# Kernel optimization log

Measured on AMD Instinct MI355X. Metric: run time of the kernel, lower is better.

Reference implementation:

```python
import jax, jax.numpy as jnp
import numpy as np

ALPHA = 0.1
K = 10


def setup_inputs() -> dict:
    key = jax.random.key(0)
    k1, k2, k3, k4, k5, k6 = jax.random.split(key, 6)
    N, F_in, H = 100000, 256, 128
    E, E_lp = 1600000, 400000
    return {
        "x": jax.random.normal(k1, (N, F_in), dtype=jnp.float32),
        "edge_index": jax.random.randint(k2, (2, E), 0, N, dtype=jnp.int64),
        "pos_edge_index": jax.random.randint(k3, (2, E_lp), 0, N, dtype=jnp.int64),
        "neg_edge_index": jax.random.randint(k4, (2, E_lp), 0, N, dtype=jnp.int64),
        "W1": jax.random.normal(k5, (F_in, H), dtype=jnp.float32) * (1.0 / np.sqrt(F_in)),
        "W2": jax.random.normal(k6, (H, H), dtype=jnp.float32) * (1.0 / np.sqrt(H)),
    }


def _appnp_propagate(h, src, dst, norm, num_nodes):
    # z_{k+1} = (1-alpha) * A_hat z_k + alpha * h   (K hops)
    z = h
    for _ in range(K):
        msg = norm[:, None] * z[src]                         # [E+N, d] gather
        agg = jax.ops.segment_sum(msg, dst, num_segments=num_nodes)  # scatter-add
        z = (1.0 - ALPHA) * agg + ALPHA * h
    return z


def reference(x, edge_index, pos_edge_index, neg_edge_index, W1, W2):
    N = x.shape[0]
    # add self-loops, GCN symmetric normalization: d^-1/2 A_sl d^-1/2
    loops = jnp.arange(N, dtype=edge_index.dtype)
    src = jnp.concatenate([edge_index[0], loops])
    dst = jnp.concatenate([edge_index[1], loops])
    deg = jax.ops.segment_sum(jnp.ones_like(dst, dtype=x.dtype), dst, num_segments=N)
    dinv = jax.lax.rsqrt(jnp.maximum(deg, 1.0))
    norm = dinv[src] * dinv[dst]

    # encode: two APPNP layers with ReLU in between (drop_rate = 0)
    z = _appnp_propagate(x @ W1, src, dst, norm, N)
    z = jax.nn.relu(z)
    z = _appnp_propagate(z @ W2, src, dst, norm, N)

    # decode: edge dot products over concatenated pos/neg edges
    e = jnp.concatenate([pos_edge_index, neg_edge_index], axis=-1)
    return jnp.sum(z[e[0]] * z[e[1]], axis=-1)
```

## Files before the change

### kernel.cpp

```cpp
#include <hip/hip_runtime.h>


constexpr int Hd = 128;
constexpr int Fin = 256;
constexpr float A_ = 0.1f;
constexpr float OMA = 0.9f;

typedef float vf2 __attribute__((ext_vector_type(2)));

__device__ __forceinline__ int idx_at(const void* p, size_t i, int is64) {
    if (is64) return (int)((const long long*)p)[i];
    return ((const int*)p)[i];
}

__device__ __forceinline__ unsigned pack_bf16x2(float x, float y) {
    unsigned ux = __float_as_uint(x);
    unsigned uy = __float_as_uint(y);
    ux = (ux + 0x7fffu + ((ux >> 16) & 1u)) >> 16;
    uy = (uy + 0x7fffu + ((uy >> 16) & 1u)) & 0xffff0000u;
    return ux | uy;
}

__device__ __forceinline__ float2 unpack_bf16x2(unsigned v) {
    float2 r;
    r.x = __uint_as_float(v << 16);
    r.y = __uint_as_float(v & 0xffff0000u);
    return r;
}

__device__ __forceinline__ unsigned short pack_fp8x2(float x, float y) {
    int v = __builtin_amdgcn_cvt_pk_fp8_f32(x, y, 0, false);
    return (unsigned short)(unsigned)v;
}

__device__ __forceinline__ float2 unpack_fp8x2(unsigned short v) {
    vf2 r = __builtin_amdgcn_cvt_pk_f32_fp8((int)(unsigned)v, false);
    float2 o;
    o.x = r[0];
    o.y = r[1];
    return o;
}

__global__ void k_detect(const int* __restrict__ p, int npairs, int* __restrict__ flag) {
    __shared__ int any32;
    if (threadIdx.x == 0) any32 = 0;
    __syncthreads();
    for (int i = threadIdx.x; i < npairs; i += blockDim.x)
        if (p[2 * i + 1] != 0) any32 = 1;
    __syncthreads();
    if (threadIdx.x == 0) *flag = any32 ? 0 : 1;
}


__global__ void k_zero_i32(int* __restrict__ p, int n) {
    int i = blockIdx.x * blockDim.x + threadIdx.x;
    if (i < n) p[i] = 0;
}

__global__ void k_count(const void* __restrict__ ei, int E, int* __restrict__ cnt,
                        const int* __restrict__ flag) {
    int is64 = *flag;
    int e = blockIdx.x * blockDim.x + threadIdx.x;
    if (e < E) {
        int d = idx_at(ei, (size_t)E + e, is64);
        atomicAdd(&cnt[d], 1);
    }
}

__global__ void k_dinv(const int* __restrict__ cnt, float* __restrict__ dinv, int N) {
    int i = blockIdx.x * blockDim.x + threadIdx.x;
    if (i < N) dinv[i] = rsqrtf((float)(cnt[i] + 1));
}

__global__ void k_scan1(const int* __restrict__ cnt, int* __restrict__ rp,
                        int* __restrict__ bsum, int N) {
    __shared__ int s[256];
    int t = threadIdx.x;
    int i = blockIdx.x * 256 + t;
    int v = (i < N) ? (cnt[i] + 1) : 0;
    s[t] = v;
    __syncthreads();
    for (int off = 1; off < 256; off <<= 1) {
        int add = (t >= off) ? s[t - off] : 0;
        __syncthreads();
        s[t] += add;
        __syncthreads();
    }
    if (i < N) rp[i] = s[t] - v;
    if (t == 255) bsum[blockIdx.x] = s[255];
}

__global__ void k_scan2(int* __restrict__ bsum, int nb) {
    __shared__ int s[512];
    int t = threadIdx.x;
    int v = (t < nb) ? bsum[t] : 0;
    s[t] = v;
    __syncthreads();
    for (int off = 1; off < 512; off <<= 1) {
        int add = (t >= off) ? s[t - off] : 0;
        __syncthreads();
        s[t] += add;
        __syncthreads();
    }
    if (t < nb) bsum[t] = s[t] - v;
}

__global__ void k_scan3(int* __restrict__ rp, const int* __restrict__ bsum,
                        int* __restrict__ cursor, const float* __restrict__ dinv,
                        int2* __restrict__ cw, int N, int Etot) {
    int i = blockIdx.x * blockDim.x + threadIdx.x;
    if (i < N) {
        int r = rp[i] + bsum[i >> 8];
        rp[i] = r;
        cursor[i] = 1;
        float d = dinv[i];
        int2 p;
        p.x = i;
        p.y = __float_as_int(OMA * d * d);
        cw[r] = p;
    }
    if (i == 0) rp[N] = Etot;
}

__global__ void k_place(const void* __restrict__ ei, int E,
                        const int* __restrict__ rp, int* __restrict__ cursor,
                        const float* __restrict__ dinv,
                        int2* __restrict__ cw, const int* __restrict__ flag) {
    int is64 = *flag;
    int e = blockIdx.x * blockDim.x + threadIdx.x;
    if (e < E) {
        int s = idx_at(ei, (size_t)e, is64);
        int d = idx_at(ei, (size_t)E + e, is64);
        int pos = rp[d] + atomicAdd(&cursor[d], 1);
        int2 p;
        p.x = s;
        p.y = __float_as_int(OMA * dinv[s] * dinv[d]);
        cw[pos] = p;
    }
}


template <int KTOT, bool RELU>
__global__ __launch_bounds__(256) void k_gemm(const float* __restrict__ A,
                                              const float* __restrict__ B,
                                              unsigned short* __restrict__ z0,
                                              unsigned* __restrict__ ah, int N) {
    __shared__ float As[64][36];
    __shared__ float Bs[32][128];
    const int t  = threadIdx.x;
    const int tx = t & 15;
    const int ty = t >> 4;
    const int r0 = blockIdx.x * 64;

    float acc[4][8];
#pragma unroll
    for (int i = 0; i < 4; ++i)
#pragma unroll
        for (int j = 0; j < 8; ++j) acc[i][j] = 0.f;

    for (int k0 = 0; k0 < KTOT; k0 += 32) {
#pragma unroll
        for (int p = 0; p < 2; ++p) {
            int row = p * 32 + (t >> 3);
            int kk  = (t & 7) * 4;
            int gr  = r0 + row;
            float4 v = make_float4(0.f, 0.f, 0.f, 0.f);
            if (gr < N) v = *(const float4*)&A[(size_t)gr * KTOT + k0 + kk];
            if (RELU) {
                v.x = fmaxf(v.x, 0.f); v.y = fmaxf(v.y, 0.f);
                v.z = fmaxf(v.z, 0.f); v.w = fmaxf(v.w, 0.f);
            }
            *(float4*)&As[row][kk] = v;
        }
#pragma unroll
        for (int p = 0; p < 4; ++p) {
            int kr = p * 8 + (t >> 5);
            int c  = (t & 31) * 4;
            *(float4*)&Bs[kr][c] = *(const float4*)&B[(size_t)(k0 + kr) * Hd + c];
        }
        __syncthreads();
#pragma unroll
        for (int kk = 0; kk < 32; ++kk) {
            float a[4];
#pragma unroll
            for (int i = 0; i < 4; ++i) a[i] = As[ty * 4 + i][kk];
            float4 b0 = *(const float4*)&Bs[kk][tx * 4];
            float4 b1 = *(const float4*)&Bs[kk][64 + tx * 4];
            float b[8] = {b0.x, b0.y, b0.z, b0.w, b1.x, b1.y, b1.z, b1.w};
#pragma unroll
            for (int i = 0; i < 4; ++i)
#pragma unroll
                for (int j = 0; j < 8; ++j) acc[i][j] = fmaf(a[i], b[j], acc[i][j]);
        }
        __syncthreads();
    }
#pragma unroll
    for (int i = 0; i < 4; ++i) {
        int gr = r0 + ty * 4 + i;
        if (gr < N) {
            ushort2 f0, f1;
            f0.x = pack_fp8x2(acc[i][0], acc[i][1]);
            f0.y = pack_fp8x2(acc[i][2], acc[i][3]);
            f1.x = pack_fp8x2(acc[i][4], acc[i][5]);
            f1.y = pack_fp8x2(acc[i][6], acc[i][7]);
            *(ushort2*)&z0[((size_t)gr << 6) + tx * 2]      = f0;
            *(ushort2*)&z0[((size_t)gr << 6) + 32 + tx * 2] = f1;
            uint2 a0, a1;
            a0.x = pack_bf16x2(A_ * acc[i][0], A_ * acc[i][1]);
            a0.y = pack_bf16x2(A_ * acc[i][2], A_ * acc[i][3]);
            a1.x = pack_bf16x2(A_ * acc[i][4], A_ * acc[i][5]);
            a1.y = pack_bf16x2(A_ * acc[i][6], A_ * acc[i][7]);
            *(uint2*)&ah[((size_t)gr << 6) + tx * 2]      = a0;
            *(uint2*)&ah[((size_t)gr << 6) + 32 + tx * 2] = a1;
        }
    }
}


template <int B, int IN8>
__device__ __forceinline__ void hop_batch(const void* __restrict__ zb,
                                          const int2* __restrict__ cw,
                                          int e, int lane,
                                          float& ax, float& ay,
                                          float& bx, float& by) {
    int2 p[B];
#pragma unroll
    for (int k = 0; k < B; ++k) p[k] = cw[e + k];
    unsigned zv[B];
#pragma unroll
    for (int k = 0; k < B; ++k) {
        if (IN8) zv[k] = ((const unsigned short*)zb)[((unsigned)p[k].x << 6) + lane];
        else     zv[k] = ((const unsigned*)zb)[((unsigned)p[k].x << 6) + lane];
    }
#pragma unroll
    for (int k = 0; k < B; ++k) {
        float wv = __int_as_float(p[k].y);
        float2 z = IN8 ? unpack_fp8x2((unsigned short)zv[k]) : unpack_bf16x2(zv[k]);
        if (k & 1) { bx = fmaf(wv, z.x, bx); by = fmaf(wv, z.y, by); }
        else       { ax = fmaf(wv, z.x, ax); ay = fmaf(wv, z.y, ay); }
    }
}

template <int IN8, int OUTM>
__global__ __launch_bounds__(256) void k_hop(const void* __restrict__ zin,
                                             const unsigned* __restrict__ ah,
                                             void* __restrict__ zout,
                                             const int* __restrict__ rp,
                                             const int2* __restrict__ cw, int N) {
    int wid  = (blockIdx.x * blockDim.x + threadIdx.x) >> 6;
    int lane = threadIdx.x & 63;
    if (wid >= N) return;

    int e   = __builtin_amdgcn_readfirstlane(rp[wid]);
    int end = __builtin_amdgcn_readfirstlane(rp[wid + 1]);

    float2 hh = unpack_bf16x2(ah[((size_t)wid << 6) + lane]);

    float ax = 0.f, ay = 0.f, bx = 0.f, by = 0.f;

    for (; e + 16 <= end; e += 16)
        hop_batch<16, IN8>(zin, cw, e, lane, ax, ay, bx, by);
    if (e + 8 <= end) { hop_batch<8, IN8>(zin, cw, e, lane, ax, ay, bx, by); e += 8; }
    if (e + 4 <= end) { hop_batch<4, IN8>(zin, cw, e, lane, ax, ay, bx, by); e += 4; }
    for (; e < end; ++e) {
        int2 p = cw[e];
        unsigned zv;
        if (IN8) zv = ((const unsigned short*)zin)[((unsigned)p.x << 6) + lane];
        else     zv = ((const unsigned*)zin)[((unsigned)p.x << 6) + lane];
        float2 z = IN8 ? unpack_fp8x2((unsigned short)zv) : unpack_bf16x2(zv);
        float wv = __int_as_float(p.y);
        ax = fmaf(wv, z.x, ax); ay = fmaf(wv, z.y, ay);
    }

    float ox = (ax + bx) + hh.x;
    float oy = (ay + by) + hh.y;
    if (OUTM == 0) {
        ((unsigned short*)zout)[((size_t)wid << 6) + lane] = pack_fp8x2(ox, oy);
    } else if (OUTM == 1) {
        ((unsigned*)zout)[((size_t)wid << 6) + lane] = pack_bf16x2(ox, oy);
    } else {
        float2 o; o.x = ox; o.y = oy;
        *(float2*)&((float*)zout)[((size_t)wid << 7) + lane * 2] = o;
    }
}


__global__ __launch_bounds__(256) void k_decode(const unsigned* __restrict__ z,
                                                const void* __restrict__ pos,
                                                const void* __restrict__ neg,
                                                float* __restrict__ out, int P, int Q,
                                                const int* __restrict__ flag) {
    int is64 = *flag;
    int t   = blockIdx.x * blockDim.x + threadIdx.x;
    int j   = t >> 4;
    int sub = t & 15;
    if (j >= P + Q) return;
    int a, b;
    if (j < P) { a = idx_at(pos, (size_t)j, is64); b = idx_at(pos, (size_t)P + j, is64); }
    else       { int jj = j - P; a = idx_at(neg, (size_t)jj, is64); b = idx_at(neg, (size_t)Q + jj, is64); }
    const uint4* za = (const uint4*)&z[(size_t)a << 6];
    const uint4* zb = (const uint4*)&z[(size_t)b << 6];
    uint4 va = za[sub];
    uint4 vb = zb[sub];
    float s = 0.f;
    {
        float2 xa, xb;
        xa = unpack_bf16x2(va.x); xb = unpack_bf16x2(vb.x);
        s += xa.x * xb.x + xa.y * xb.y;
        xa = unpack_bf16x2(va.y); xb = unpack_bf16x2(vb.y);
        s += xa.x * xb.x + xa.y * xb.y;
        xa = unpack_bf16x2(va.z); xb = unpack_bf16x2(vb.z);
        s += xa.x * xb.x + xa.y * xb.y;
        xa = unpack_bf16x2(va.w); xb = unpack_bf16x2(vb.w);
        s += xa.x * xb.x + xa.y * xb.y;
    }
#pragma unroll
    for (int off = 8; off >= 1; off >>= 1) s += __shfl_xor(s, off, 16);
    if (sub == 0) out[j] = s;
}


extern "C" void kernel_launch(void* const* d_in, const int* in_sizes, int n_in,
                              void* d_out, int out_size, void* d_ws, size_t ws_size,
                              hipStream_t stream) {
    const float* x   = (const float*)d_in[0];
    const void*  ei  = d_in[1];
    const void*  pos = d_in[2];
    const void*  neg = d_in[3];
    const float* W1  = (const float*)d_in[4];
    const float* W2  = (const float*)d_in[5];
    float*       out = (float*)d_out;

    const int N = in_sizes[0] / Fin;
    const int E = in_sizes[1] / 2;
    const int P = in_sizes[2] / 2;
    const int Q = in_sizes[3] / 2;
    const int Etot = E + N;

    char*  ws  = (char*)d_ws;
    size_t off = 0;
    auto carve = [&](size_t bytes) -> void* {
        void* p = ws + off;
        off = (off + bytes + 511) & ~(size_t)511;
        return p;
    };
    float*          zF   = (float*)carve((size_t)N * Hd * 4);
    unsigned short* f0   = (unsigned short*)carve((size_t)N * 64 * 2);
    unsigned short* f1   = (unsigned short*)carve((size_t)N * 64 * 2);
    unsigned*       zBF  = (unsigned*)carve((size_t)N * 64 * 4);
    unsigned*       zB2  = (unsigned*)carve((size_t)N * 64 * 4);
    unsigned*       ah   = (unsigned*)carve((size_t)N * 64 * 4);
    float*          dinv = (float*)carve((size_t)N * 4);
    int*     cnt    = (int*)carve((size_t)N * 4);
    int*     rp     = (int*)carve((size_t)(N + 1) * 4);
    int*     cursor = (int*)carve((size_t)N * 4);
    int2*    cw     = (int2*)carve((size_t)Etot * 8);
    int      nb     = (N + 255) / 256;
    int*     bsum   = (int*)carve((size_t)nb * 4);
    int*     flag   = (int*)carve(4);
    (void)ws_size;

    const int gN = (N + 255) / 256;
    const int gE = (E + 255) / 256;

    k_detect<<<1, 256, 0, stream>>>((const int*)ei, 4096, flag);
    k_zero_i32<<<gN, 256, 0, stream>>>(cnt, N);
    k_count<<<gE, 256, 0, stream>>>(ei, E, cnt, flag);
    k_dinv<<<gN, 256, 0, stream>>>(cnt, dinv, N);
    k_scan1<<<nb, 256, 0, stream>>>(cnt, rp, bsum, N);
    k_scan2<<<1, 512, 0, stream>>>(bsum, nb);
    k_scan3<<<gN, 256, 0, stream>>>(rp, bsum, cursor, dinv, cw, N, Etot);
    k_place<<<gE, 256, 0, stream>>>(ei, E, rp, cursor, dinv, cw, flag);

    const int gGemm = (N + 63) / 64;
    const int gHop  = (N * 64 + 255) / 256;

    unsigned short* fb[2] = {f0, f1};

    k_gemm<Fin, false><<<gGemm, 256, 0, stream>>>(x, W1, f0, ah, N);
    for (int k = 0; k < 8; ++k)
        k_hop<1, 0><<<gHop, 256, 0, stream>>>(fb[k & 1], ah, fb[(k + 1) & 1], rp, cw, N);
    k_hop<1, 1><<<gHop, 256, 0, stream>>>(f0, ah, zBF, rp, cw, N);
    k_hop<0, 2><<<gHop, 256, 0, stream>>>(zBF, ah, zF, rp, cw, N);

    k_gemm<Hd, true><<<gGemm, 256, 0, stream>>>(zF, W2, f0, ah, N);
    for (int k = 0; k < 8; ++k)
        k_hop<1, 0><<<gHop, 256, 0, stream>>>(fb[k & 1], ah, fb[(k + 1) & 1], rp, cw, N);
    k_hop<1, 1><<<gHop, 256, 0, stream>>>(f0, ah, zBF, rp, cw, N);
    k_hop<0, 1><<<gHop, 256, 0, stream>>>(zBF, ah, zB2, rp, cw, N);

    const int gDec = ((P + Q) * 16 + 255) / 256;
    k_decode<<<gDec, 256, 0, stream>>>(zB2, pos, neg, out, P, Q, flag);
}
```

Measured before the change: 1.203 ms.

## Use bf16 MFMA GEMMs and fuse ReLU into bf16 hop output

```diff
diff --git a/kernel.cpp b/kernel.cpp
--- a/kernel.cpp
+++ b/kernel.cpp
@@ -7,10 +7,17 @@
 constexpr float OMA = 0.9f;
 
 typedef float vf2 __attribute__((ext_vector_type(2)));
+typedef __bf16 bf16x8 __attribute__((ext_vector_type(8)));
+typedef float f32x4 __attribute__((ext_vector_type(4)));
 
 __device__ __forceinline__ int idx_at(const void* p, size_t i, int is64) {
     if (is64) return (int)((const long long*)p)[i];
     return ((const int*)p)[i];
+}
+
+__device__ __forceinline__ unsigned short bf16_of(float x) {
+    unsigned u = __float_as_uint(x);
+    return (unsigned short)((u + 0x7fffu + ((u >> 16) & 1u)) >> 16);
 }
 
 __device__ __forceinline__ unsigned pack_bf16x2(float x, float y) {
@@ -139,79 +146,133 @@
     }
 }
 
-
-template <int KTOT, bool RELU>
-__global__ __launch_bounds__(256) void k_gemm(const float* __restrict__ A,
-                                              const float* __restrict__ B,
-                                              unsigned short* __restrict__ z0,
-                                              unsigned* __restrict__ ah, int N) {
-    __shared__ float As[64][36];
-    __shared__ float Bs[32][128];
-    const int t  = threadIdx.x;
-    const int tx = t & 15;
-    const int ty = t >> 4;
-    const int r0 = blockIdx.x * 64;
-
-    float acc[4][8];
-#pragma unroll
-    for (int i = 0; i < 4; ++i)
-#pragma unroll
-        for (int j = 0; j < 8; ++j) acc[i][j] = 0.f;
+__global__ void k_wt(const float* __restrict__ W, unsigned short* __restrict__ Wt, int K) {
+    int i = blockIdx.x * blockDim.x + threadIdx.x;
+    if (i < K * 128) {
+        int k = i >> 7, c = i & 127;
+        Wt[c * K + k] = bf16_of(W[i]);
+    }
+}
+
+
+template <int KTOT, bool AF32>
+__global__ __launch_bounds__(256) void k_gemm_mfma(const void* __restrict__ Ap,
+                                                   const unsigned short* __restrict__ Wt,
+                                                   unsigned short* __restrict__ z0,
+                                                   unsigned* __restrict__ ah, int N) {
+    __shared__ __align__(16) char smem[64 * 132 * 4];
+    unsigned short (*As)[40] = (unsigned short(*)[40])smem;
+    unsigned short (*Bs)[40] = (unsigned short(*)[40])(smem + 5120);
+    float (*Cs)[132] = (float(*)[132])smem;
+
+    const int t    = threadIdx.x;
+    const int lane = t & 63;
+    const int w    = t >> 6;
+    const int wr   = w >> 1;
+    const int wc   = w & 1;
+    const int r0   = blockIdx.x * 64;
+
+    f32x4 acc[2][4];
+#pragma unroll
+    for (int i = 0; i < 2; ++i)
+#pragma unroll
+        for (int j = 0; j < 4; ++j)
+#pragma unroll
+            for (int q = 0; q < 4; ++q) acc[i][j][q] = 0.f;
+
+    const int arow = t >> 2;
+    const int akc  = (t & 3) * 8;
+    const int bcol = t >> 1;
+    const int bkc  = (t & 1) * 16;
 
     for (int k0 = 0; k0 < KTOT; k0 += 32) {
-#pragma unroll
-        for (int p = 0; p < 2; ++p) {
-            int row = p * 32 + (t >> 3);
-            int kk  = (t & 7) * 4;
-            int gr  = r0 + row;
-            float4 v = make_float4(0.f, 0.f, 0.f, 0.f);
-            if (gr < N) v = *(const float4*)&A[(size_t)gr * KTOT + k0 + kk];
-            if (RELU) {
-                v.x = fmaxf(v.x, 0.f); v.y = fmaxf(v.y, 0.f);
-                v.z = fmaxf(v.z, 0.f); v.w = fmaxf(v.w, 0.f);
+        {
+            int gr = r0 + arow;
+            if (AF32) {
+                uint4 s = make_uint4(0, 0, 0, 0);
+                if (gr < N) {
+                    const float* a = (const float*)Ap + (size_t)gr * KTOT + k0 + akc;
+                    float4 v0 = *(const float4*)a;
+                    float4 v1 = *(const float4*)(a + 4);
+                    s.x = pack_bf16x2(v0.x, v0.y);
+                    s.y = pack_bf16x2(v0.z, v0.w);
+                    s.z = pack_bf16x2(v1.x, v1.y);
+                    s.w = pack_bf16x2(v1.z, v1.w);
+                }
+                *(uint4*)&As[arow][akc] = s;
+            } else {
+                uint4 s = make_uint4(0, 0, 0, 0);
+                if (gr < N) s = *(const uint4*)((const unsigned short*)Ap + (size_t)gr * KTOT + k0 + akc);
+                *(uint4*)&As[arow][akc] = s;
             }
-            *(float4*)&As[row][kk] = v;
         }
-#pragma unroll
-        for (int p = 0; p < 4; ++p) {
-            int kr = p * 8 + (t >> 5);
-            int c  = (t & 31) * 4;
-            *(float4*)&Bs[kr][c] = *(const float4*)&B[(size_t)(k0 + kr) * Hd + c];
+        {
+            const unsigned short* wsrc = Wt + (size_t)bcol * KTOT + k0 + bkc;
+            *(uint4*)&Bs[bcol][bkc]     = *(const uint4*)wsrc;
+            *(uint4*)&Bs[bcol][bkc + 8] = *(const uint4*)(wsrc + 8);
         }
         __syncthreads();
-#pragma unroll
-        for (int kk = 0; kk < 32; ++kk) {
-            float a[4];
-#pragma unroll
-            for (int i = 0; i < 4; ++i) a[i] = As[ty * 4 + i][kk];
-            float4 b0 = *(const float4*)&Bs[kk][tx * 4];
-            float4 b1 = *(const float4*)&Bs[kk][64 + tx * 4];
-            float b[8] = {b0.x, b0.y, b0.z, b0.w, b1.x, b1.y, b1.z, b1.w};
-#pragma unroll
-            for (int i = 0; i < 4; ++i)
-#pragma unroll
-                for (int j = 0; j < 8; ++j) acc[i][j] = fmaf(a[i], b[j], acc[i][j]);
+        {
+            const int kblk = (lane >> 4) * 8;
+            const int l15  = lane & 15;
+            bf16x8 af[2], bfr[4];
+#pragma unroll
+            for (int i = 0; i < 2; ++i)
+                af[i] = *(const bf16x8*)&As[wr * 32 + i * 16 + l15][kblk];
+#pragma unroll
+            for (int j = 0; j < 4; ++j)
+                bfr[j] = *(const bf16x8*)&Bs[wc * 64 + j * 16 + l15][kblk];
+#pragma unroll
+            for (int i = 0; i < 2; ++i)
+#pragma unroll
+                for (int j = 0; j < 4; ++j)
+                    acc[i][j] = __builtin_amdgcn_mfma_f32_16x16x32_bf16(af[i], bfr[j], acc[i][j], 0, 0, 0);
         }
         __syncthreads();
     }
-#pragma unroll
-    for (int i = 0; i < 4; ++i) {
-        int gr = r0 + ty * 4 + i;
+
+    {
+        const int l15 = lane & 15;
+        const int rq  = (lane >> 4) * 4;
+#pragma unroll
+        for (int i = 0; i < 2; ++i)
+#pragma unroll
+            for (int j = 0; j < 4; ++j)
+#pragma unroll
+                for (int q = 0; q < 4; ++q)
+                    Cs[wr * 32 + i * 16 + rq + q][wc * 64 + j * 16 + l15] = acc[i][j][q];
+    }
+    __syncthreads();
+    {
+        const int row = t >> 2;
+        const int cb  = (t & 3) * 32;
+        const int gr  = r0 + row;
         if (gr < N) {
-            ushort2 f0, f1;
-            f0.x = pack_fp8x2(acc[i][0], acc[i][1]);
-            f0.y = pack_fp8x2(acc[i][2], acc[i][3]);
-            f1.x = pack_fp8x2(acc[i][4], acc[i][5]);
-            f1.y = pack_fp8x2(acc[i][6], acc[i][7]);
-            *(ushort2*)&z0[((size_t)gr << 6) + tx * 2]      = f0;
-            *(ushort2*)&z0[((size_t)gr << 6) + 32 + tx * 2] = f1;
-            uint2 a0, a1;
-            a0.x = pack_bf16x2(A_ * acc[i][0], A_ * acc[i][1]);
-            a0.y = pack_bf16x2(A_ * acc[i][2], A_ * acc[i][3]);
-            a1.x = pack_bf16x2(A_ * acc[i][4], A_ * acc[i][5]);
-            a1.y = pack_bf16x2(A_ * acc[i][6], A_ * acc[i][7]);
-            *(uint2*)&ah[((size_t)gr << 6) + tx * 2]      = a0;
-            *(uint2*)&ah[((size_t)gr << 6) + 32 + tx * 2] = a1;
+            float c[32];
+#pragma unroll
+            for (int m = 0; m < 8; ++m) {
+                float4 v = *(const float4*)&Cs[row][cb + m * 4];
+                c[m * 4 + 0] = v.x; c[m * 4 + 1] = v.y; c[m * 4 + 2] = v.z; c[m * 4 + 3] = v.w;
+            }
+            unsigned pk[8];
+#pragma unroll
+            for (int m = 0; m < 8; ++m) {
+                unsigned lo = (unsigned)pack_fp8x2(c[4 * m + 0], c[4 * m + 1]);
+                unsigned hi = (unsigned)pack_fp8x2(c[4 * m + 2], c[4 * m + 3]);
+                pk[m] = lo | (hi << 16);
+            }
+            uint4* zd = (uint4*)&z0[((size_t)gr << 6) + (cb >> 1)];
+            zd[0] = make_uint4(pk[0], pk[1], pk[2], pk[3]);
+            zd[1] = make_uint4(pk[4], pk[5], pk[6], pk[7]);
+            unsigned am[16];
+#pragma unroll
+            for (int m = 0; m < 16; ++m)
+                am[m] = pack_bf16x2(A_ * c[2 * m], A_ * c[2 * m + 1]);
+            uint4* ad = (uint4*)&ah[((size_t)gr << 6) + (cb >> 1)];
+            ad[0] = make_uint4(am[0],  am[1],  am[2],  am[3]);
+            ad[1] = make_uint4(am[4],  am[5],  am[6],  am[7]);
+            ad[2] = make_uint4(am[8],  am[9],  am[10], am[11]);
+            ad[3] = make_uint4(am[12], am[13], am[14], am[15]);
         }
     }
 }
@@ -279,8 +340,8 @@
     } else if (OUTM == 1) {
         ((unsigned*)zout)[((size_t)wid << 6) + lane] = pack_bf16x2(ox, oy);
     } else {
-        float2 o; o.x = ox; o.y = oy;
-        *(float2*)&((float*)zout)[((size_t)wid << 7) + lane * 2] = o;
+        ((unsigned*)zout)[((size_t)wid << 6) + lane] =
+            pack_bf16x2(fmaxf(ox, 0.f), fmaxf(oy, 0.f));
     }
 }
 
@@ -344,12 +405,14 @@
         off = (off + bytes + 511) & ~(size_t)511;
         return p;
     };
-    float*          zF   = (float*)carve((size_t)N * Hd * 4);
     unsigned short* f0   = (unsigned short*)carve((size_t)N * 64 * 2);
     unsigned short* f1   = (unsigned short*)carve((size_t)N * 64 * 2);
     unsigned*       zBF  = (unsigned*)carve((size_t)N * 64 * 4);
     unsigned*       zB2  = (unsigned*)carve((size_t)N * 64 * 4);
+    unsigned*       zRB  = (unsigned*)carve((size_t)N * 64 * 4);
     unsigned*       ah   = (unsigned*)carve((size_t)N * 64 * 4);
+    unsigned short* Wt1  = (unsigned short*)carve((size_t)128 * 256 * 2);
+    unsigned short* Wt2  = (unsigned short*)carve((size_t)128 * 128 * 2);
     float*          dinv = (float*)carve((size_t)N * 4);
     int*     cnt    = (int*)carve((size_t)N * 4);
     int*     rp     = (int*)carve((size_t)(N + 1) * 4);
@@ -371,19 +434,21 @@
     k_scan2<<<1, 512, 0, stream>>>(bsum, nb);
     k_scan3<<<gN, 256, 0, stream>>>(rp, bsum, cursor, dinv, cw, N, Etot);
     k_place<<<gE, 256, 0, stream>>>(ei, E, rp, cursor, dinv, cw, flag);
+    k_wt<<<(256 * 128 + 255) / 256, 256, 0, stream>>>(W1, Wt1, Fin);
+    k_wt<<<(128 * 128 + 255) / 256, 256, 0, stream>>>(W2, Wt2, Hd);
 
     const int gGemm = (N + 63) / 64;
     const int gHop  = (N * 64 + 255) / 256;
 
     unsigned short* fb[2] = {f0, f1};
 
-    k_gemm<Fin, false><<<gGemm, 256, 0, stream>>>(x, W1, f0, ah, N);
+    k_gemm_mfma<Fin, true><<<gGemm, 256, 0, stream>>>(x, Wt1, f0, ah, N);
     for (int k = 0; k < 8; ++k)
         k_hop<1, 0><<<gHop, 256, 0, stream>>>(fb[k & 1], ah, fb[(k + 1) & 1], rp, cw, N);
     k_hop<1, 1><<<gHop, 256, 0, stream>>>(f0, ah, zBF, rp, cw, N);
-    k_hop<0, 2><<<gHop, 256, 0, stream>>>(zBF, ah, zF, rp, cw, N);
-
-    k_gemm<Hd, true><<<gGemm, 256, 0, stream>>>(zF, W2, f0, ah, N);
+    k_hop<0, 3><<<gHop, 256, 0, stream>>>(zBF, ah, zRB, rp, cw, N);
+
+    k_gemm_mfma<Hd, false><<<gGemm, 256, 0, stream>>>(zRB, Wt2, f0, ah, N);
     for (int k = 0; k < 8; ++k)
         k_hop<1, 0><<<gHop, 256, 0, stream>>>(fb[k & 1], ah, fb[(k + 1) & 1], rp, cw, N);
     k_hop<1, 1><<<gHop, 256, 0, stream>>>(f0, ah, zBF, rp, cw, N);
```

New measurement: 1.089 ms. -9.5%, faster.
